# Kernel optimization log

Measured on AMD Instinct MI355X. Metric: run time of the kernel, lower is better.

The kernel has to match this reference:

```python
import jax, jax.numpy as jnp
import numpy as np

EMBED_DIM = 1024
NUM_HEADS = 16
HEAD_DIM = EMBED_DIM // NUM_HEADS
B, T = 2, 2048


def setup_inputs() -> dict:
    key = jax.random.key(0)
    ks = jax.random.split(key, 9)
    s = 1.0 / np.sqrt(EMBED_DIM)
    x = jax.random.normal(ks[0], (B, T, EMBED_DIM), dtype=jnp.float32)
    Wq = jax.random.uniform(ks[1], (EMBED_DIM, EMBED_DIM), jnp.float32, -s, s)
    bq = jax.random.uniform(ks[2], (EMBED_DIM,), jnp.float32, -s, s)
    Wk = jax.random.uniform(ks[3], (EMBED_DIM, EMBED_DIM), jnp.float32, -s, s)
    bk = jax.random.uniform(ks[4], (EMBED_DIM,), jnp.float32, -s, s)
    Wv = jax.random.uniform(ks[5], (EMBED_DIM, EMBED_DIM), jnp.float32, -s, s)
    bv = jax.random.uniform(ks[6], (EMBED_DIM,), jnp.float32, -s, s)
    Wo = jax.random.uniform(ks[7], (EMBED_DIM, EMBED_DIM), jnp.float32, -s, s)
    bo = jax.random.uniform(ks[8], (EMBED_DIM,), jnp.float32, -s, s)
    return {"x": x, "Wq": Wq, "bq": bq, "Wk": Wk, "bk": bk,
            "Wv": Wv, "bv": bv, "Wo": Wo, "bo": bo}


def reference(x, Wq, bq, Wk, bk, Wv, bv, Wo, bo):
    Bx, Tx, D = x.shape
    # projections (torch Linear: y = x @ W^T + b); here W stored as [in, out]
    q = (x @ Wq + bq).reshape(Bx, Tx, NUM_HEADS, HEAD_DIM).transpose(0, 2, 1, 3)
    k = (x @ Wk + bk).reshape(Bx, Tx, NUM_HEADS, HEAD_DIM).transpose(0, 2, 1, 3)
    v = (x @ Wv + bv).reshape(Bx, Tx, NUM_HEADS, HEAD_DIM).transpose(0, 2, 1, 3)
    scale = HEAD_DIM ** -0.5
    attn = jnp.einsum('bhqd,bhkd->bhqk', q, k) * scale  # [B, H, T, T]
    causal = jnp.tril(jnp.ones((Tx, Tx), dtype=bool))
    attn = jnp.where(causal[None, None], attn, -jnp.inf)
    attn = jax.nn.softmax(attn, axis=-1)
    out = jnp.einsum('bhqk,bhkd->bhqd', attn, v)  # [B, H, T, hd]
    out = out.transpose(0, 2, 1, 3).reshape(Bx, Tx, D)
    return out @ Wo + bo
```

## Files before the change

kernel.cpp:

```cpp
#include <hip/hip_runtime.h>

#define EMBED 1024
#define NHEADS 16
#define HDIM 64
#define SEQ 2048
#define BATCH 2
#define MROWS (BATCH * SEQ)

using bf16x8 = __attribute__((ext_vector_type(8))) short;
using f32x4  = __attribute__((ext_vector_type(4))) float;
using us4    = __attribute__((ext_vector_type(4))) unsigned short;

__device__ __forceinline__ unsigned short f2bf(float f) {
    unsigned int u = __builtin_bit_cast(unsigned int, f);
    u = (u + 0x7fffu + ((u >> 16) & 1u)) >> 16;
    return (unsigned short)u;
}

__device__ __forceinline__ void async16(const unsigned short* g, unsigned short* l) {
    __builtin_amdgcn_global_load_lds(
        (const __attribute__((address_space(1))) void*)g,
        (__attribute__((address_space(3))) void*)l, 16, 0, 0);
}

__global__ __launch_bounds__(256)
void cvt_x(const float* __restrict__ in, unsigned short* __restrict__ out)
{
    int i = blockIdx.x * 256 + threadIdx.x;
    float4 v = ((const float4*)in)[i];
    us4 o;
    o[0] = f2bf(v.x); o[1] = f2bf(v.y); o[2] = f2bf(v.z); o[3] = f2bf(v.w);
    ((us4*)out)[i] = o;
}

__global__ __launch_bounds__(256)
void cvt_w(const float* __restrict__ W0, const float* __restrict__ W1,
           const float* __restrict__ W2, const float* __restrict__ W3,
           unsigned short* __restrict__ T0, unsigned short* __restrict__ T1,
           unsigned short* __restrict__ T2, unsigned short* __restrict__ T3)
{
    const float* W = blockIdx.z == 0 ? W0 : blockIdx.z == 1 ? W1 :
                     blockIdx.z == 2 ? W2 : W3;
    unsigned short* T = blockIdx.z == 0 ? T0 : blockIdx.z == 1 ? T1 :
                        blockIdx.z == 2 ? T2 : T3;
    __shared__ unsigned short tile[64][72];
    const int tid = threadIdx.x;
    const int k0 = blockIdx.y << 6, n0 = blockIdx.x << 6;
    const int lr = tid >> 4, lc = (tid & 15) << 2;
#pragma unroll
    for (int it = 0; it < 4; ++it) {
        int kr = lr + it * 16;
        float4 v = *(const float4*)(W + (size_t)(k0 + kr) * EMBED + n0 + lc);
        tile[lc + 0][kr] = f2bf(v.x);
        tile[lc + 1][kr] = f2bf(v.y);
        tile[lc + 2][kr] = f2bf(v.z);
        tile[lc + 3][kr] = f2bf(v.w);
    }
    __syncthreads();
#pragma unroll
    for (int it = 0; it < 4; ++it) {
        int nr = lr + it * 16;
        us4 o = *(const us4*)(&tile[nr][lc]);
        *(us4*)(T + (size_t)(n0 + nr) * EMBED + k0 + lc) = o;
    }
}

__device__ __forceinline__ void mfma_gemm_core(
    const unsigned short* __restrict__ A, const unsigned short* __restrict__ Bt,
    int bm, int n0, unsigned short* As, unsigned short* Bs,
    int wv, int lane, f32x4 acc[4][4])
{
    const int m16 = lane & 15, quad = lane >> 4;
    const int mb = (wv >> 1) << 6;
    const int nb = (wv & 1) << 6;

    const unsigned short* ga = A  + (size_t)(bm + wv * 32 + (lane >> 3)) * EMBED + ((lane & 7) << 3);
    const unsigned short* gb = Bt + (size_t)(n0 + wv * 32 + (lane >> 3)) * EMBED + ((lane & 7) << 3);
    unsigned short* la = As + wv * 32 * 64;
    unsigned short* lb = Bs + wv * 32 * 64;

    for (int k0 = 0; k0 < EMBED; k0 += 64) {
        __syncthreads();
#pragma unroll
        for (int j = 0; j < 4; ++j) {
            async16(ga + j * 8 * EMBED, la + j * 8 * 64);
            async16(gb + j * 8 * EMBED, lb + j * 8 * 64);
        }
        ga += 64; gb += 64;
        __syncthreads();
#pragma unroll
        for (int ks = 0; ks < 2; ++ks) {
            const int ko = ks * 32 + (quad << 3);
            bf16x8 af[4], bfv[4];
#pragma unroll
            for (int i = 0; i < 4; ++i) {
                af[i]  = *(const bf16x8*)(As + (mb + i * 16 + m16) * 64 + ko);
                bfv[i] = *(const bf16x8*)(Bs + (nb + i * 16 + m16) * 64 + ko);
            }
#pragma unroll
            for (int i = 0; i < 4; ++i)
#pragma unroll
                for (int j = 0; j < 4; ++j)
                    acc[i][j] = __builtin_amdgcn_mfma_f32_16x16x32_bf16(
                        af[i], bfv[j], acc[i][j], 0, 0, 0);
        }
    }
}

__device__ __forceinline__ void mfma_gemm_core64(
    const unsigned short* __restrict__ A, const unsigned short* __restrict__ Bt,
    int bm, int n0, unsigned short* As, unsigned short* Bs,
    int wv, int lane, f32x4 acc[4][2])
{
    const int m16 = lane & 15, quad = lane >> 4;
    const int mb = (wv >> 1) << 6;
    const int nb = (wv & 1) << 5;

    const unsigned short* ga = A  + (size_t)(bm + wv * 32 + (lane >> 3)) * EMBED + ((lane & 7) << 3);
    const unsigned short* gb = Bt + (size_t)(n0 + wv * 16 + (lane >> 3)) * EMBED + ((lane & 7) << 3);
    unsigned short* la = As + wv * 32 * 64;
    unsigned short* lb = Bs + wv * 16 * 64;

    for (int k0 = 0; k0 < EMBED; k0 += 64) {
        __syncthreads();
#pragma unroll
        for (int j = 0; j < 4; ++j)
            async16(ga + j * 8 * EMBED, la + j * 8 * 64);
#pragma unroll
        for (int j = 0; j < 2; ++j)
            async16(gb + j * 8 * EMBED, lb + j * 8 * 64);
        ga += 64; gb += 64;
        __syncthreads();
#pragma unroll
        for (int ks = 0; ks < 2; ++ks) {
            const int ko = ks * 32 + (quad << 3);
            bf16x8 af[4], bfv[2];
#pragma unroll
            for (int i = 0; i < 4; ++i)
                af[i] = *(const bf16x8*)(As + (mb + i * 16 + m16) * 64 + ko);
#pragma unroll
            for (int j = 0; j < 2; ++j)
                bfv[j] = *(const bf16x8*)(Bs + (nb + j * 16 + m16) * 64 + ko);
#pragma unroll
            for (int i = 0; i < 4; ++i)
#pragma unroll
                for (int j = 0; j < 2; ++j)
                    acc[i][j] = __builtin_amdgcn_mfma_f32_16x16x32_bf16(
                        af[i], bfv[j], acc[i][j], 0, 0, 0);
        }
    }
}

__global__ __launch_bounds__(256)
void qkv_gemm(const unsigned short* __restrict__ xb,
              const unsigned short* __restrict__ Wtq,
              const unsigned short* __restrict__ Wtk,
              const unsigned short* __restrict__ Wtv,
              const float* __restrict__ bq, const float* __restrict__ bk,
              const float* __restrict__ bv,
              unsigned short* __restrict__ Qo, unsigned short* __restrict__ Ko,
              unsigned short* __restrict__ Vto)
{
    __shared__ __align__(16) unsigned short As[128 * 64];
    __shared__ __align__(16) unsigned short Bs[128 * 64];
    const int tid = threadIdx.x, wv = tid >> 6, lane = tid & 63;
    const int m16 = lane & 15, quad = lane >> 4;
    const int which = blockIdx.x >> 3;
    const int n0 = (blockIdx.x & 7) << 7;
    const int bm = blockIdx.y << 7;
    const unsigned short* Bt = which == 0 ? Wtq : which == 1 ? Wtk : Wtv;
    const float* bias = which == 0 ? bq : which == 1 ? bk : bv;

    f32x4 acc[4][4];
#pragma unroll
    for (int i = 0; i < 4; ++i)
#pragma unroll
        for (int j = 0; j < 4; ++j) acc[i][j] = (f32x4){0.f, 0.f, 0.f, 0.f};

    mfma_gemm_core(xb, Bt, bm, n0, As, Bs, wv, lane, acc);

    const int mb = (wv >> 1) << 6, nb = (wv & 1) << 6;
    const float qscale = 0.125f * 1.4426950408889634f;
#pragma unroll
    for (int i = 0; i < 4; ++i) {
        const int m0 = bm + mb + i * 16 + quad * 4;
        const int b = m0 >> 11, t0 = m0 & (SEQ - 1);
#pragma unroll
        for (int j = 0; j < 4; ++j) {
            const int n = n0 + nb + j * 16 + m16;
            const int h = n >> 6, d = n & 63;
            const float bval = bias[n];
            if (which == 2) {
                us4 v;
#pragma unroll
                for (int r = 0; r < 4; ++r) v[r] = f2bf(acc[i][j][r] + bval);
                *(us4*)(Vto + ((((size_t)(b * NHEADS + h)) << 6) + d) * SEQ + t0) = v;
            } else {
                const float sc = which == 0 ? qscale : 1.f;
                unsigned short* dst = (which == 0 ? Qo : Ko) +
                    ((((size_t)(b * NHEADS + h)) << 11) + t0) * 64 + d;
#pragma unroll
                for (int r = 0; r < 4; ++r)
                    dst[(size_t)r * 64] = f2bf((acc[i][j][r] + bval) * sc);
            }
        }
    }
}

__global__ __launch_bounds__(256)
void out_gemm(const unsigned short* __restrict__ aob,
              const unsigned short* __restrict__ Wto,
              const float* __restrict__ bo, float* __restrict__ out)
{
    __shared__ __align__(16) unsigned short As[128 * 64];
    __shared__ __align__(16) unsigned short Bs[64 * 64];
    const int tid = threadIdx.x, wv = tid >> 6, lane = tid & 63;
    const int m16 = lane & 15, quad = lane >> 4;
    const int n0 = blockIdx.x << 6;
    const int bm = blockIdx.y << 7;

    f32x4 acc[4][2];
#pragma unroll
    for (int i = 0; i < 4; ++i)
#pragma unroll
        for (int j = 0; j < 2; ++j) acc[i][j] = (f32x4){0.f, 0.f, 0.f, 0.f};

    mfma_gemm_core64(aob, Wto, bm, n0, As, Bs, wv, lane, acc);

    const int mb = (wv >> 1) << 6, nb = (wv & 1) << 5;
#pragma unroll
    for (int i = 0; i < 4; ++i) {
        const int m0 = bm + mb + i * 16 + quad * 4;
#pragma unroll
        for (int j = 0; j < 2; ++j) {
            const int n = n0 + nb + j * 16 + m16;
            const float bval = bo[n];
#pragma unroll
            for (int r = 0; r < 4; ++r)
                out[(size_t)(m0 + r) * EMBED + n] = acc[i][j][r] + bval;
        }
    }
}

__global__ __launch_bounds__(256)
void attn_mfma(const unsigned short* __restrict__ Qb,
               const unsigned short* __restrict__ Kb,
               const unsigned short* __restrict__ Vtb,
               unsigned short* __restrict__ Oout)
{
    __shared__ __align__(16) unsigned short Ks[2][64 * 72];
    __shared__ __align__(16) unsigned short Vt[2][64 * 72];
    __shared__ __align__(16) unsigned short Ps[4][16 * 72];

    const int tid  = threadIdx.x;
    const int wv   = tid >> 6;
    const int lane = tid & 63;
    const int m16  = lane & 15;
    const int quad = lane >> 4;
    const int bh   = blockIdx.y;
    const int b    = bh >> 4, h = bh & 15;

    const int srow = tid >> 2;
    const int scol = (tid & 3) << 4;

    bf16x8 rk0, rk1, rv0, rv1;
    auto load_tile = [&](int k0) {
        const unsigned short* sk = Kb + (((size_t)bh << 11) + k0 + srow) * 64 + scol;
        rk0 = *(const bf16x8*)sk;
        rk1 = *(const bf16x8*)(sk + 8);
        const unsigned short* sv = Vtb + (((size_t)bh << 6) + srow) * SEQ + k0 + scol;
        rv0 = *(const bf16x8*)sv;
        rv1 = *(const bf16x8*)(sv + 8);
    };

    for (int phase = 0; phase < 2; ++phase) {
        const int qt = phase == 0 ? (31 - (int)blockIdx.x) : (int)blockIdx.x;
        const int q0 = qt << 6;

        const size_t qoff =
            (((size_t)bh << 11) + q0 + (wv << 4) + m16) * 64 + (quad << 3);
        bf16x8 qa0 = *(const bf16x8*)(Qb + qoff);
        bf16x8 qa1 = *(const bf16x8*)(Qb + qoff + 32);

        f32x4 o[4];
#pragma unroll
        for (int dt = 0; dt < 4; ++dt) o[dt] = (f32x4){0.f, 0.f, 0.f, 0.f};
        float m_ = -1e30f, l_ = 0.f;

        load_tile(0);
        __syncthreads();

        for (int kt = 0; kt <= qt; ++kt) {
            unsigned short* Kp = Ks[kt & 1];
            unsigned short* Vp = Vt[kt & 1];
            *(bf16x8*)(Kp + srow * 72 + scol)     = rk0;
            *(bf16x8*)(Kp + srow * 72 + scol + 8) = rk1;
            *(bf16x8*)(Vp + srow * 72 + scol)     = rv0;
            *(bf16x8*)(Vp + srow * 72 + scol + 8) = rv1;
            __syncthreads();
            if (kt < qt) load_tile((kt + 1) << 6);

            const bool diag = (kt == qt);

            f32x4 s[4];
#pragma unroll
            for (int g = 0; g < 4; ++g) {
                if (diag && g > wv) {
                    s[g] = (f32x4){-1e30f, -1e30f, -1e30f, -1e30f};
                    continue;
                }
                const unsigned short* kp = Kp + (g * 16 + m16) * 72 + (quad << 3);
                bf16x8 kb0 = *(const bf16x8*)kp;
                bf16x8 kb1 = *(const bf16x8*)(kp + 32);
                s[g] = (f32x4){0.f, 0.f, 0.f, 0.f};
                s[g] = __builtin_amdgcn_mfma_f32_16x16x32_bf16(kb0, qa0, s[g], 0, 0, 0);
                s[g] = __builtin_amdgcn_mfma_f32_16x16x32_bf16(kb1, qa1, s[g], 0, 0, 0);
            }
            if (diag) {
#pragma unroll
                for (int r = 0; r < 4; ++r)
                    if (quad * 4 + r > m16) s[wv][r] = -1e30f;
            }

            float mx = s[0][0];
#pragma unroll
            for (int g = 0; g < 4; ++g)
#pragma unroll
                for (int r = 0; r < 4; ++r) mx = fmaxf(mx, s[g][r]);
            mx = fmaxf(mx, __shfl_xor(mx, 16));
            mx = fmaxf(mx, __shfl_xor(mx, 32));
            const float nm = fmaxf(m_, mx);
            const float alpha = exp2f(m_ - nm);
            float sum = 0.f;
#pragma unroll
            for (int g = 0; g < 4; ++g)
#pragma unroll
                for (int r = 0; r < 4; ++r) {
                    float p = exp2f(s[g][r] - nm);
                    s[g][r] = p;
                    sum += p;
                }
            sum += __shfl_xor(sum, 16);
            sum += __shfl_xor(sum, 32);
            l_ = l_ * alpha + sum;
            m_ = nm;

#pragma unroll
            for (int g = 0; g < 4; ++g) {
                us4 pv;
#pragma unroll
                for (int r = 0; r < 4; ++r) pv[r] = f2bf(s[g][r]);
                *(us4*)(&Ps[wv][m16 * 72 + g * 16 + quad * 4]) = pv;
            }

#pragma unroll
            for (int dt = 0; dt < 4; ++dt) o[dt] *= alpha;

            const unsigned short* pp = &Ps[wv][m16 * 72 + (quad << 3)];
            bf16x8 pa0 = *(const bf16x8*)pp;
            bf16x8 pa1 = *(const bf16x8*)(pp + 32);
            const bool skip_hi = diag && (wv < 2);
#pragma unroll
            for (int dt = 0; dt < 4; ++dt) {
                const unsigned short* vp = Vp + (dt * 16 + m16) * 72 + (quad << 3);
                bf16x8 vb0 = *(const bf16x8*)vp;
                o[dt] = __builtin_amdgcn_mfma_f32_16x16x32_bf16(vb0, pa0, o[dt], 0, 0, 0);
                if (!skip_hi) {
                    bf16x8 vb1 = *(const bf16x8*)(vp + 32);
                    o[dt] = __builtin_amdgcn_mfma_f32_16x16x32_bf16(vb1, pa1, o[dt], 0, 0, 0);
                }
            }
        }

        const float inv = 1.f / l_;
        const int t = q0 + (wv << 4) + m16;
        unsigned short* dst =
            Oout + ((size_t)((b << 11) + t) << 10) + (h << 6) + (quad << 2);
#pragma unroll
        for (int dt = 0; dt < 4; ++dt) {
            us4 w;
#pragma unroll
            for (int r = 0; r < 4; ++r) w[r] = f2bf(o[dt][r] * inv);
            *(us4*)(dst + dt * 16) = w;
        }
    }
}

extern "C" void kernel_launch(void* const* d_in, const int* in_sizes, int n_in,
                              void* d_out, int out_size, void* d_ws, size_t ws_size,
                              hipStream_t stream) {
    const float* x  = (const float*)d_in[0];
    const float* Wq = (const float*)d_in[1];
    const float* bq = (const float*)d_in[2];
    const float* Wk = (const float*)d_in[3];
    const float* bk = (const float*)d_in[4];
    const float* Wv = (const float*)d_in[5];
    const float* bv = (const float*)d_in[6];
    const float* Wo = (const float*)d_in[7];
    const float* bo = (const float*)d_in[8];
    float* out = (float*)d_out;

    const size_t HSZ = (size_t)MROWS * EMBED;
    const size_t WSZ = (size_t)EMBED * EMBED;
    unsigned short* qb  = (unsigned short*)d_ws;
    unsigned short* kb  = qb + HSZ;
    unsigned short* vtb = kb + HSZ;
    unsigned short* aob = vtb + HSZ;
    unsigned short* xb  = aob + HSZ;
    unsigned short* wtq = xb + HSZ;
    unsigned short* wtk = wtq + WSZ;
    unsigned short* wtv = wtk + WSZ;
    unsigned short* wto = wtv + WSZ;

    cvt_x<<<MROWS * EMBED / 1024, 256, 0, stream>>>(x, xb);
    cvt_w<<<dim3(16, 16, 4), 256, 0, stream>>>(Wq, Wk, Wv, Wo, wtq, wtk, wtv, wto);

    qkv_gemm<<<dim3(24, 32), 256, 0, stream>>>(xb, wtq, wtk, wtv, bq, bk, bv,
                                               qb, kb, vtb);

    attn_mfma<<<dim3(16, BATCH * NHEADS), 256, 0, stream>>>(qb, kb, vtb, aob);

    out_gemm<<<dim3(16, 32), 256, 0, stream>>>(aob, wto, bo, out);
}
```

Baseline: 226.2 us.

## Split attention into one query tile per block with XOR-swizzled LDS and lazy rescale

The attention kernel now launches one block per (batch-head, query tile), 1024 blocks, instead of each block handling two paired tiles in sequence. Query tiles are ordered so that consecutive blocks interleave short and long causal rows. LDS tiles drop the 72-element padding in favour of an XOR swizzle. The softmax rescales the accumulator only when the running max grows by more than 8, and packs bf16 with v_cvt_pk_bf16_f32. This aims at more parallelism, fewer bank conflicts and fewer ALU ops, at the cost of losing the balanced per-block work pairing and of running softmax against a stale max.

Result: faster. 213.8 us (-5.5%).

```diff
diff --git a/kernel.cpp b/kernel.cpp
--- a/kernel.cpp
+++ b/kernel.cpp
@@ -10,11 +10,18 @@
 using bf16x8 = __attribute__((ext_vector_type(8))) short;
 using f32x4  = __attribute__((ext_vector_type(4))) float;
 using us4    = __attribute__((ext_vector_type(4))) unsigned short;
+using u32x2  = __attribute__((ext_vector_type(2))) unsigned int;
 
 __device__ __forceinline__ unsigned short f2bf(float f) {
     unsigned int u = __builtin_bit_cast(unsigned int, f);
     u = (u + 0x7fffu + ((u >> 16) & 1u)) >> 16;
     return (unsigned short)u;
+}
+
+__device__ __forceinline__ unsigned int cvt_pk_bf16(float a, float b) {
+    unsigned int d;
+    asm("v_cvt_pk_bf16_f32 %0, %1, %2" : "=v"(d) : "v"(a), "v"(b));
+    return d;
 }
 
 __device__ __forceinline__ void async16(const unsigned short* g, unsigned short* l) {
@@ -248,23 +255,30 @@
                const unsigned short* __restrict__ Vtb,
                unsigned short* __restrict__ Oout)
 {
-    __shared__ __align__(16) unsigned short Ks[2][64 * 72];
-    __shared__ __align__(16) unsigned short Vt[2][64 * 72];
-    __shared__ __align__(16) unsigned short Ps[4][16 * 72];
+    __shared__ __align__(16) unsigned short Ks[2][64 * 64];
+    __shared__ __align__(16) unsigned short Vt[2][64 * 64];
+    __shared__ __align__(16) unsigned short Ps[4][16 * 64];
 
     const int tid  = threadIdx.x;
     const int wv   = tid >> 6;
     const int lane = tid & 63;
     const int m16  = lane & 15;
     const int quad = lane >> 4;
-    const int bh   = blockIdx.y;
+    const int bh   = blockIdx.x;
     const int b    = bh >> 4, h = bh & 15;
 
+    const int yr = blockIdx.y & 7, yk = blockIdx.y >> 3;
+    const int qt = yk == 0 ? yr : yk == 1 ? 15 - yr : yk == 2 ? 16 + yr : 31 - yr;
+    const int q0 = qt << 6;
+
     const int srow = tid >> 2;
-    const int scol = (tid & 3) << 4;
+    const int cc   = tid & 3;
+    const int swr  = srow & 7;
+    const int sx   = m16 & 7;
 
     bf16x8 rk0, rk1, rv0, rv1;
     auto load_tile = [&](int k0) {
+        const int scol = cc << 4;
         const unsigned short* sk = Kb + (((size_t)bh << 11) + k0 + srow) * 64 + scol;
         rk0 = *(const bf16x8*)sk;
         rk1 = *(const bf16x8*)(sk + 8);
@@ -273,116 +287,120 @@
         rv1 = *(const bf16x8*)(sv + 8);
     };
 
-    for (int phase = 0; phase < 2; ++phase) {
-        const int qt = phase == 0 ? (31 - (int)blockIdx.x) : (int)blockIdx.x;
-        const int q0 = qt << 6;
-
-        const size_t qoff =
-            (((size_t)bh << 11) + q0 + (wv << 4) + m16) * 64 + (quad << 3);
-        bf16x8 qa0 = *(const bf16x8*)(Qb + qoff);
-        bf16x8 qa1 = *(const bf16x8*)(Qb + qoff + 32);
-
-        f32x4 o[4];
-#pragma unroll
-        for (int dt = 0; dt < 4; ++dt) o[dt] = (f32x4){0.f, 0.f, 0.f, 0.f};
-        float m_ = -1e30f, l_ = 0.f;
-
-        load_tile(0);
+    const size_t qoff =
+        (((size_t)bh << 11) + q0 + (wv << 4) + m16) * 64 + (quad << 3);
+    bf16x8 qa0 = *(const bf16x8*)(Qb + qoff);
+    bf16x8 qa1 = *(const bf16x8*)(Qb + qoff + 32);
+
+    f32x4 o[4];
+#pragma unroll
+    for (int dt = 0; dt < 4; ++dt) o[dt] = (f32x4){0.f, 0.f, 0.f, 0.f};
+    float m_ = -1e30f, l_ = 0.f;
+
+    load_tile(0);
+
+    for (int kt = 0; kt <= qt; ++kt) {
+        unsigned short* Kp = Ks[kt & 1];
+        unsigned short* Vp = Vt[kt & 1];
+        {
+            unsigned short* kd = Kp + srow * 64;
+            unsigned short* vd = Vp + srow * 64;
+            *(bf16x8*)(kd + (((2 * cc) ^ swr) << 3))     = rk0;
+            *(bf16x8*)(kd + (((2 * cc + 1) ^ swr) << 3)) = rk1;
+            *(bf16x8*)(vd + (((2 * cc) ^ swr) << 3))     = rv0;
+            *(bf16x8*)(vd + (((2 * cc + 1) ^ swr) << 3)) = rv1;
+        }
         __syncthreads();
-
-        for (int kt = 0; kt <= qt; ++kt) {
-            unsigned short* Kp = Ks[kt & 1];
-            unsigned short* Vp = Vt[kt & 1];
-            *(bf16x8*)(Kp + srow * 72 + scol)     = rk0;
-            *(bf16x8*)(Kp + srow * 72 + scol + 8) = rk1;
-            *(bf16x8*)(Vp + srow * 72 + scol)     = rv0;
-            *(bf16x8*)(Vp + srow * 72 + scol + 8) = rv1;
-            __syncthreads();
-            if (kt < qt) load_tile((kt + 1) << 6);
-
-            const bool diag = (kt == qt);
-
-            f32x4 s[4];
+        if (kt < qt) load_tile((kt + 1) << 6);
+
+        const bool diag = (kt == qt);
+
+        f32x4 s[4];
+#pragma unroll
+        for (int g = 0; g < 4; ++g) {
+            if (diag && g > wv) {
+                s[g] = (f32x4){-1e30f, -1e30f, -1e30f, -1e30f};
+                continue;
+            }
+            const unsigned short* kr = Kp + (g * 16 + m16) * 64;
+            bf16x8 kb0 = *(const bf16x8*)(kr + ((quad ^ sx) << 3));
+            bf16x8 kb1 = *(const bf16x8*)(kr + (((quad + 4) ^ sx) << 3));
+            s[g] = (f32x4){0.f, 0.f, 0.f, 0.f};
+            s[g] = __builtin_amdgcn_mfma_f32_16x16x32_bf16(kb0, qa0, s[g], 0, 0, 0);
+            s[g] = __builtin_amdgcn_mfma_f32_16x16x32_bf16(kb1, qa1, s[g], 0, 0, 0);
+        }
+        if (diag) {
+#pragma unroll
+            for (int r = 0; r < 4; ++r)
+                if (quad * 4 + r > m16) s[wv][r] = -1e30f;
+        }
+
+        float mx = fmaxf(fmaxf(s[0][0], s[0][1]), fmaxf(s[0][2], s[0][3]));
+#pragma unroll
+        for (int g = 1; g < 4; ++g)
+            mx = fmaxf(mx, fmaxf(fmaxf(s[g][0], s[g][1]), fmaxf(s[g][2], s[g][3])));
+        mx = fmaxf(mx, __shfl_xor(mx, 16));
+        mx = fmaxf(mx, __shfl_xor(mx, 32));
+
+        if (mx > m_ + 8.f) {
+            const float alpha = exp2f(m_ - mx);
+            m_ = mx;
+            l_ *= alpha;
+#pragma unroll
+            for (int dt = 0; dt < 4; ++dt) o[dt] *= alpha;
+        }
+
+        float sum = 0.f;
+        unsigned int pw0[4], pw1[4];
+#pragma unroll
+        for (int g = 0; g < 4; ++g) {
+            float p0 = exp2f(s[g][0] - m_);
+            float p1 = exp2f(s[g][1] - m_);
+            float p2 = exp2f(s[g][2] - m_);
+            float p3 = exp2f(s[g][3] - m_);
+            sum += (p0 + p1) + (p2 + p3);
+            pw0[g] = cvt_pk_bf16(p0, p1);
+            pw1[g] = cvt_pk_bf16(p2, p3);
+        }
+        sum += __shfl_xor(sum, 16);
+        sum += __shfl_xor(sum, 32);
+        l_ += sum;
+
+        {
+            unsigned short* pd = Ps[wv] + m16 * 64 + ((quad & 1) << 2);
 #pragma unroll
             for (int g = 0; g < 4; ++g) {
-                if (diag && g > wv) {
-                    s[g] = (f32x4){-1e30f, -1e30f, -1e30f, -1e30f};
-                    continue;
-                }
-                const unsigned short* kp = Kp + (g * 16 + m16) * 72 + (quad << 3);
-                bf16x8 kb0 = *(const bf16x8*)kp;
-                bf16x8 kb1 = *(const bf16x8*)(kp + 32);
-                s[g] = (f32x4){0.f, 0.f, 0.f, 0.f};
-                s[g] = __builtin_amdgcn_mfma_f32_16x16x32_bf16(kb0, qa0, s[g], 0, 0, 0);
-                s[g] = __builtin_amdgcn_mfma_f32_16x16x32_bf16(kb1, qa1, s[g], 0, 0, 0);
+                u32x2 w; w.x = pw0[g]; w.y = pw1[g];
+                *(u32x2*)(pd + (((2 * g + (quad >> 1)) ^ sx) << 3)) = w;
             }
-            if (diag) {
-#pragma unroll
-                for (int r = 0; r < 4; ++r)
-                    if (quad * 4 + r > m16) s[wv][r] = -1e30f;
+        }
+
+        const unsigned short* pr = Ps[wv] + m16 * 64;
+        bf16x8 pa0 = *(const bf16x8*)(pr + ((quad ^ sx) << 3));
+        bf16x8 pa1 = *(const bf16x8*)(pr + (((quad + 4) ^ sx) << 3));
+        const bool skip_hi = diag && (wv < 2);
+#pragma unroll
+        for (int dt = 0; dt < 4; ++dt) {
+            const unsigned short* vr = Vp + (dt * 16 + m16) * 64;
+            bf16x8 vb0 = *(const bf16x8*)(vr + ((quad ^ sx) << 3));
+            o[dt] = __builtin_amdgcn_mfma_f32_16x16x32_bf16(vb0, pa0, o[dt], 0, 0, 0);
+            if (!skip_hi) {
+                bf16x8 vb1 = *(const bf16x8*)(vr + (((quad + 4) ^ sx) << 3));
+                o[dt] = __builtin_amdgcn_mfma_f32_16x16x32_bf16(vb1, pa1, o[dt], 0, 0, 0);
             }
-
-            float mx = s[0][0];
-#pragma unroll
-            for (int g = 0; g < 4; ++g)
-#pragma unroll
-                for (int r = 0; r < 4; ++r) mx = fmaxf(mx, s[g][r]);
-            mx = fmaxf(mx, __shfl_xor(mx, 16));
-            mx = fmaxf(mx, __shfl_xor(mx, 32));
-            const float nm = fmaxf(m_, mx);
-            const float alpha = exp2f(m_ - nm);
-            float sum = 0.f;
-#pragma unroll
-            for (int g = 0; g < 4; ++g)
-#pragma unroll
-                for (int r = 0; r < 4; ++r) {
-                    float p = exp2f(s[g][r] - nm);
-                    s[g][r] = p;
-                    sum += p;
-                }
-            sum += __shfl_xor(sum, 16);
-            sum += __shfl_xor(sum, 32);
-            l_ = l_ * alpha + sum;
-            m_ = nm;
-
-#pragma unroll
-            for (int g = 0; g < 4; ++g) {
-                us4 pv;
-#pragma unroll
-                for (int r = 0; r < 4; ++r) pv[r] = f2bf(s[g][r]);
-                *(us4*)(&Ps[wv][m16 * 72 + g * 16 + quad * 4]) = pv;
-            }
-
-#pragma unroll
-            for (int dt = 0; dt < 4; ++dt) o[dt] *= alpha;
-
-            const unsigned short* pp = &Ps[wv][m16 * 72 + (quad << 3)];
-            bf16x8 pa0 = *(const bf16x8*)pp;
-            bf16x8 pa1 = *(const bf16x8*)(pp + 32);
-            const bool skip_hi = diag && (wv < 2);
-#pragma unroll
-            for (int dt = 0; dt < 4; ++dt) {
-                const unsigned short* vp = Vp + (dt * 16 + m16) * 72 + (quad << 3);
-                bf16x8 vb0 = *(const bf16x8*)vp;
-                o[dt] = __builtin_amdgcn_mfma_f32_16x16x32_bf16(vb0, pa0, o[dt], 0, 0, 0);
-                if (!skip_hi) {
-                    bf16x8 vb1 = *(const bf16x8*)(vp + 32);
-                    o[dt] = __builtin_amdgcn_mfma_f32_16x16x32_bf16(vb1, pa1, o[dt], 0, 0, 0);
-                }
-            }
-        }
-
-        const float inv = 1.f / l_;
-        const int t = q0 + (wv << 4) + m16;
-        unsigned short* dst =
-            Oout + ((size_t)((b << 11) + t) << 10) + (h << 6) + (quad << 2);
-#pragma unroll
-        for (int dt = 0; dt < 4; ++dt) {
-            us4 w;
-#pragma unroll
-            for (int r = 0; r < 4; ++r) w[r] = f2bf(o[dt][r] * inv);
-            *(us4*)(dst + dt * 16) = w;
-        }
+        }
+    }
+
+    const float inv = 1.f / l_;
+    const int t = q0 + (wv << 4) + m16;
+    unsigned short* dst =
+        Oout + ((size_t)((b << 11) + t) << 10) + (h << 6) + (quad << 2);
+#pragma unroll
+    for (int dt = 0; dt < 4; ++dt) {
+        u32x2 w;
+        w.x = cvt_pk_bf16(o[dt][0] * inv, o[dt][1] * inv);
+        w.y = cvt_pk_bf16(o[dt][2] * inv, o[dt][3] * inv);
+        *(u32x2*)(dst + dt * 16) = w;
     }
 }
 
@@ -418,7 +436,7 @@
     qkv_gemm<<<dim3(24, 32), 256, 0, stream>>>(xb, wtq, wtk, wtv, bq, bk, bv,
                                                qb, kb, vtb);
 
-    attn_mfma<<<dim3(16, BATCH * NHEADS), 256, 0, stream>>>(qb, kb, vtb, aob);
+    attn_mfma<<<dim3(32, 32), 256, 0, stream>>>(qb, kb, vtb, aob);
 
     out_gemm<<<dim3(16, 32), 256, 0, stream>>>(aob, wto, bo, out);
 }
```
